# Optimization experiments

Hardware: AMD Instinct MI355X
Metric: run time of the kernel (lower is better)

## Reference

```python
import jax, jax.numpy as jnp
import numpy as np

B, N, C_IN, C_OUT, CHEB_K, EMB = 32, 2048, 128, 128, 3, 128
LN_EPS = 1e-12


def setup_inputs() -> dict:
    key = jax.random.key(0)
    k0, k1, k2, k3 = jax.random.split(key, 4)
    return {
        "x": jax.random.normal(k0, (B, N, C_IN), dtype=jnp.float32),
        "node_embeddings": jax.random.normal(k1, (N, EMB), dtype=jnp.float32),
        "weights_pool": jax.random.normal(k2, (EMB, CHEB_K, C_IN, C_OUT), dtype=jnp.float32) * 0.02,
        "bias_pool": jax.random.normal(k3, (EMB, C_OUT), dtype=jnp.float32) * 0.02,
        "ln_gamma": jnp.ones((EMB,), dtype=jnp.float32),
        "ln_beta": jnp.zeros((EMB,), dtype=jnp.float32),
    }


def reference(x, node_embeddings, weights_pool, bias_pool, ln_gamma, ln_beta):
    # x: [B, N, C_in]; node_embeddings: [N, D]
    cheb_k = weights_pool.shape[1]
    n = node_embeddings.shape[0]

    # LayerNorm over embed dim (biased variance, eps=1e-12); dropout is eval-mode identity
    mu = jnp.mean(node_embeddings, axis=-1, keepdims=True)
    var = jnp.mean(jnp.square(node_embeddings - mu), axis=-1, keepdims=True)
    e = (node_embeddings - mu) * jax.lax.rsqrt(var + LN_EPS) * ln_gamma + ln_beta

    # Adaptive adjacency: softmax(elu(E E^T)) over last dim (mask=None path)
    supports = jax.nn.softmax(jax.nn.elu(e @ e.T), axis=-1)  # [N, N]

    # Chebyshev polynomial set: T0=I, T1=A, Tk = 2A Tk-1 - Tk-2
    s_list = [jnp.eye(n, dtype=x.dtype), supports]
    for _ in range(2, cheb_k):
        s_list.append(2.0 * supports @ s_list[-1] - s_list[-2])
    S = jnp.stack(s_list, axis=0)  # [K, N, N]

    # Hypernetwork: per-node weights and bias
    weights = jnp.einsum("nd,dkio->nkio", e, weights_pool)  # [N, K, C_in, C_out]
    bias = e @ bias_pool  # [N, C_out]

    # Graph conv: gather neighborhoods per Chebyshev order, then per-node GEMM
    x_g = jnp.einsum("knm,bmc->bnkc", S, x)  # [B, N, K, C_in]
    out = jnp.einsum("bnki,nkio->bno", x_g, weights) + bias  # [B, N, C_out]
    return out
```

## Files before the change

### kernel.cpp

```cpp
#include <hip/hip_runtime.h>

#define DI __device__ __forceinline__

typedef unsigned short u16;
typedef short short8 __attribute__((ext_vector_type(8)));
typedef float f32x4 __attribute__((ext_vector_type(4)));
typedef u16 u16x4 __attribute__((ext_vector_type(4)));

#define NN 2048
#define CC 128
#define BB 32
#define DD 128
#define OO 128
#define KI 384
#define JJ 49152

DI u16 f2bf(float f) {
  union { float f; unsigned u; } v; v.f = f;
  return (u16)((v.u + 0x7fffu + ((v.u >> 16) & 1u)) >> 16);
}
DI float bf2f(u16 h) {
  union { unsigned u; float f; } v; v.u = ((unsigned)h) << 16;
  return v.f;
}

typedef __attribute__((address_space(3))) unsigned int lds_u32;
typedef __attribute__((address_space(1))) unsigned int glob_u32;

DI void gl16(const void* g, void* l) {
  __builtin_amdgcn_global_load_lds((const glob_u32*)g, (lds_u32*)l, 16, 0, 0);
}

__global__ __launch_bounds__(128)
void k_ln(const float* __restrict__ emb, const float* __restrict__ gam,
          const float* __restrict__ bet, float* __restrict__ e,
          u16* __restrict__ ehi, u16* __restrict__ elo) {
  __shared__ float s2[2], q2[2];
  const int n = blockIdx.x, t = threadIdx.x;
  const float v = emb[(size_t)n * DD + t];
  float s = v;
  #pragma unroll
  for (int off = 32; off; off >>= 1) s += __shfl_down(s, off);
  if ((t & 63) == 0) s2[t >> 6] = s;
  __syncthreads();
  const float mu = (s2[0] + s2[1]) * (1.f / 128.f);
  const float dv = v - mu;
  float q = dv * dv;
  #pragma unroll
  for (int off = 32; off; off >>= 1) q += __shfl_down(q, off);
  if ((t & 63) == 0) q2[t >> 6] = q;
  __syncthreads();
  const float var = (q2[0] + q2[1]) * (1.f / 128.f);
  const float ev = dv * rsqrtf(var + 1e-12f) * gam[t] + bet[t];
  e[(size_t)n * DD + t] = ev;
  const u16 hi = f2bf(ev);
  ehi[(size_t)n * DD + t] = hi;
  elo[(size_t)n * DD + t] = f2bf(ev - bf2f(hi));
}

__global__ __launch_bounds__(256, 2)
void k_zg(const u16* __restrict__ ehi, const u16* __restrict__ elo, float* __restrict__ Z) {
  __shared__ char smem[32768];
  const int t = threadIdx.x;
  const int w = t >> 6, l = t & 63;
  const int l15 = l & 15, kg = l >> 4;
  const int wr = (w >> 1) * 64, wc = (w & 1) * 64;
  const int row0 = blockIdx.x * 128, col0 = blockIdx.y * 128;

  f32x4 acc[4][4];
  #pragma unroll
  for (int i = 0; i < 4; ++i)
    #pragma unroll
    for (int j = 0; j < 4; ++j) { f32x4 z = {0.f, 0.f, 0.f, 0.f}; acc[i][j] = z; }

  const int ra = t >> 3, sa = t & 7;
  #pragma unroll 1
  for (int it = 0; it < 6; ++it) {
    const int term = it >> 1;
    const int k0 = (it & 1) * 64;
    const u16* As = (term == 2) ? elo : ehi;
    const u16* Bs = (term == 1) ? elo : ehi;
    __syncthreads();
    #pragma unroll
    for (int i = 0; i < 4; ++i) {
      const int r = i * 32 + ra;
      const int ss = sa ^ (r & 7);
      gl16(As + (size_t)(row0 + r) * DD + k0 + ss * 8, smem + i * 4096 + t * 16);
      gl16(Bs + (size_t)(col0 + r) * DD + k0 + ss * 8, smem + 16384 + i * 4096 + t * 16);
    }
    __syncthreads();
    short8 af[2][4], bfv[2][4];
    #pragma unroll
    for (int mt = 0; mt < 4; ++mt) {
      const int row = wr + mt * 16 + l15;
      #pragma unroll
      for (int ks = 0; ks < 2; ++ks) {
        const int sl = (ks * 4 + kg) ^ (row & 7);
        af[ks][mt] = *(const short8*)(smem + row * 128 + sl * 16);
      }
    }
    #pragma unroll
    for (int nt = 0; nt < 4; ++nt) {
      const int row = wc + nt * 16 + l15;
      #pragma unroll
      for (int ks = 0; ks < 2; ++ks) {
        const int sl = (ks * 4 + kg) ^ (row & 7);
        bfv[ks][nt] = *(const short8*)(smem + 16384 + row * 128 + sl * 16);
      }
    }
    #pragma unroll
    for (int ks = 0; ks < 2; ++ks)
      #pragma unroll
      for (int mt = 0; mt < 4; ++mt)
        #pragma unroll
        for (int nt = 0; nt < 4; ++nt)
          acc[mt][nt] = __builtin_amdgcn_mfma_f32_16x16x32_bf16(af[ks][mt], bfv[ks][nt], acc[mt][nt], 0, 0, 0);
  }
  #pragma unroll
  for (int mt = 0; mt < 4; ++mt) {
    const int n_ = row0 + wr + mt * 16 + kg * 4;
    #pragma unroll
    for (int nt = 0; nt < 4; ++nt) {
      const int m_ = col0 + wc + nt * 16 + l15;
      #pragma unroll
      for (int r = 0; r < 4; ++r) {
        const float v = acc[mt][nt][r];
        Z[(size_t)(n_ + r) * NN + m_] = (v > 0.f) ? v : expm1f(v);
      }
    }
  }
}

__global__ __launch_bounds__(256)
void k_sm(const float* __restrict__ Z, u16* __restrict__ Abf) {
  __shared__ float red[4];
  const int n = blockIdx.x, t = threadIdx.x, w = t >> 6;
  const float* zr = Z + (size_t)n * NN + t * 8;
  float4 v0 = *(const float4*)(zr);
  float4 v1 = *(const float4*)(zr + 4);
  float z[8] = {v0.x, v0.y, v0.z, v0.w, v1.x, v1.y, v1.z, v1.w};
  float mx = z[0];
  #pragma unroll
  for (int i = 1; i < 8; ++i) mx = fmaxf(mx, z[i]);
  #pragma unroll
  for (int off = 32; off; off >>= 1) mx = fmaxf(mx, __shfl_xor(mx, off));
  if ((t & 63) == 0) red[w] = mx;
  __syncthreads();
  mx = fmaxf(fmaxf(red[0], red[1]), fmaxf(red[2], red[3]));
  __syncthreads();
  float sm = 0.f;
  #pragma unroll
  for (int i = 0; i < 8; ++i) { z[i] = expf(z[i] - mx); sm += z[i]; }
  #pragma unroll
  for (int off = 32; off; off >>= 1) sm += __shfl_xor(sm, off);
  if ((t & 63) == 0) red[w] = sm;
  __syncthreads();
  const float inv = 1.f / (red[0] + red[1] + red[2] + red[3]);
  short8 pk;
  #pragma unroll
  for (int i = 0; i < 8; ++i) pk[i] = (short)f2bf(z[i] * inv);
  *(short8*)(Abf + (size_t)n * NN + t * 8) = pk;
}

__global__ __launch_bounds__(256)
void k_tc(const float* __restrict__ x, u16* __restrict__ xt, u16* __restrict__ xbf) {
  __shared__ float ld[64 * 68];
  const int t = threadIdx.x;
  const int m0 = blockIdx.x * 64, c0 = blockIdx.y * 64, b = blockIdx.z;
  const float* xb = x + (size_t)b * NN * CC;
  u16* xfb = xbf + (size_t)b * NN * CC;
  #pragma unroll
  for (int i = 0; i < 4; ++i) {
    const int m = i * 16 + (t >> 4), c4 = (t & 15) * 4;
    const float4 v = *(const float4*)&xb[(size_t)(m0 + m) * CC + c0 + c4];
    *(float4*)&ld[m * 68 + c4] = v;
    u16x4 cv = { f2bf(v.x), f2bf(v.y), f2bf(v.z), f2bf(v.w) };
    *(u16x4*)&xfb[(size_t)(m0 + m) * CC + c0 + c4] = cv;
  }
  __syncthreads();
  u16* xtb = xt + (size_t)b * CC * NN;
  #pragma unroll
  for (int i = 0; i < 4; ++i) {
    const int c = i * 16 + (t >> 4), m4 = (t & 15) * 4;
    u16x4 v = { f2bf(ld[(m4 + 0) * 68 + c]), f2bf(ld[(m4 + 1) * 68 + c]),
                f2bf(ld[(m4 + 2) * 68 + c]), f2bf(ld[(m4 + 3) * 68 + c]) };
    *(u16x4*)&xtb[(size_t)(c0 + c) * NN + m0 + m4] = v;
  }
}

__global__ __launch_bounds__(256)
void k_wpt(const float* __restrict__ wp, u16* __restrict__ wpt) {
  __shared__ float ld[64 * 68];
  const int t = threadIdx.x;
  const int d0 = blockIdx.x * 64, o0 = blockIdx.y * 64, ki = blockIdx.z;
  #pragma unroll
  for (int i = 0; i < 4; ++i) {
    const int d = i * 16 + (t >> 4), o4 = (t & 15) * 4;
    *(float4*)&ld[d * 68 + o4] = *(const float4*)&wp[((size_t)(d0 + d) * KI + ki) * OO + o0 + o4];
  }
  __syncthreads();
  #pragma unroll
  for (int i = 0; i < 4; ++i) {
    const int o = i * 16 + (t >> 4), d4 = (t & 15) * 4;
    u16x4 v = { f2bf(ld[(d4 + 0) * 68 + o]), f2bf(ld[(d4 + 1) * 68 + o]),
                f2bf(ld[(d4 + 2) * 68 + o]), f2bf(ld[(d4 + 3) * 68 + o]) };
    *(u16x4*)&wpt[((size_t)(o0 + o) * KI + ki) * DD + d0 + d4] = v;
  }
}

__global__ __launch_bounds__(128)
void k_bias(const float* __restrict__ e, const float* __restrict__ bp, float* __restrict__ bias) {
  const int n = blockIdx.x, o = threadIdx.x;
  const float* er = e + (size_t)n * DD;
  float acc = 0.f;
  for (int d = 0; d < 128; ++d) acc = fmaf(er[d], bp[(size_t)d * OO + o], acc);
  bias[(size_t)n * OO + o] = acc;
}

template<int MODE>
__global__ __launch_bounds__(256, 2)
void gemm_bf16(const u16* __restrict__ Ab, int lda,
               const u16* __restrict__ Bb, int ldb, int ksteps,
               u16* __restrict__ out0, u16* __restrict__ out1,
               const u16* __restrict__ xaux) {
  __shared__ char smem[34816];
  const int t = threadIdx.x;
  const int w = t >> 6, l = t & 63;
  const int l15 = l & 15, kg = l >> 4;
  const int wr = (w >> 1) * 64, wc = (w & 1) * 64;

  const u16 *Abase, *Bbase;
  int row0 = 0, col0 = 0, b = 0;
  if constexpr (MODE == 0 || MODE == 1) {
    const int lin = blockIdx.x + (int)gridDim.x * blockIdx.y;
    const int xcd = lin & 7, pos = lin >> 3;
    const int tile = xcd * 2 + (pos & 1);
    b = pos >> 1;
    if constexpr (MODE == 0) {
      row0 = tile * 128;
      Abase = Ab + (size_t)row0 * lda;
      Bbase = Bb + (size_t)b * CC * NN;
    } else {
      col0 = tile * 128;
      Abase = Ab + (size_t)b * CC * NN;
      Bbase = Bb + (size_t)col0 * NN;
    }
  } else {
    row0 = blockIdx.x * 128; col0 = blockIdx.y * 128;
    Abase = Ab + (size_t)row0 * 128;
    Bbase = Bb + (size_t)col0 * 128;
  }

  f32x4 acc[4][4];
  #pragma unroll
  for (int i = 0; i < 4; ++i)
    #pragma unroll
    for (int j = 0; j < 4; ++j) { f32x4 z = {0.f, 0.f, 0.f, 0.f}; acc[i][j] = z; }

  const int ra = t >> 3, sa = t & 7;
  for (int kt = 0; kt < ksteps; ++kt) {
    const int k0 = kt * 64;
    __syncthreads();
    #pragma unroll
    for (int i = 0; i < 4; ++i) {
      const int r = i * 32 + ra;
      const int ss = sa ^ (r & 7);
      gl16(Abase + (size_t)r * lda + k0 + ss * 8, smem + i * 4096 + t * 16);
    }
    #pragma unroll
    for (int i = 0; i < 4; ++i) {
      const int r = i * 32 + ra;
      const int ss = sa ^ (r & 7);
      gl16(Bbase + (size_t)r * ldb + k0 + ss * 8, smem + 16384 + i * 4096 + t * 16);
    }
    __syncthreads();
    short8 af[2][4], bfv[2][4];
    #pragma unroll
    for (int mt = 0; mt < 4; ++mt) {
      const int row = wr + mt * 16 + l15;
      #pragma unroll
      for (int ks = 0; ks < 2; ++ks) {
        const int sl = (ks * 4 + kg) ^ (row & 7);
        af[ks][mt] = *(const short8*)(smem + row * 128 + sl * 16);
      }
    }
    #pragma unroll
    for (int nt = 0; nt < 4; ++nt) {
      const int row = wc + nt * 16 + l15;
      #pragma unroll
      for (int ks = 0; ks < 2; ++ks) {
        const int sl = (ks * 4 + kg) ^ (row & 7);
        bfv[ks][nt] = *(const short8*)(smem + 16384 + row * 128 + sl * 16);
      }
    }
    #pragma unroll
    for (int ks = 0; ks < 2; ++ks)
      #pragma unroll
      for (int mt = 0; mt < 4; ++mt)
        #pragma unroll
        for (int nt = 0; nt < 4; ++nt)
          acc[mt][nt] = __builtin_amdgcn_mfma_f32_16x16x32_bf16(af[ks][mt], bfv[ks][nt], acc[mt][nt], 0, 0, 0);
  }

  if constexpr (MODE == 0) {
    u16* y1t = out0 + (size_t)b * CC * NN;
    #pragma unroll
    for (int mt = 0; mt < 4; ++mt) {
      const int n_ = row0 + wr + mt * 16 + kg * 4;
      #pragma unroll
      for (int nt = 0; nt < 4; ++nt) {
        const int c_ = wc + nt * 16 + l15;
        u16x4 v = { f2bf(acc[mt][nt][0]), f2bf(acc[mt][nt][1]),
                    f2bf(acc[mt][nt][2]), f2bf(acc[mt][nt][3]) };
        *(u16x4*)(y1t + (size_t)c_ * NN + n_) = v;
      }
    }
    __syncthreads();
    u16* L = (u16*)smem;
    #pragma unroll
    for (int mt = 0; mt < 4; ++mt) {
      const int nl = wr + mt * 16 + kg * 4;
      #pragma unroll
      for (int nt = 0; nt < 4; ++nt) {
        const int c_ = wc + nt * 16 + l15;
        #pragma unroll
        for (int r = 0; r < 4; ++r) L[(nl + r) * 136 + c_] = f2bf(acc[mt][nt][r]);
      }
    }
    __syncthreads();
    u16* y1o = out1 + (size_t)b * NN * CC;
    const int nl2 = t >> 1, ch = (t & 1) * 64;
    #pragma unroll
    for (int q = 0; q < 8; ++q) {
      short8 vv = *(const short8*)(L + nl2 * 136 + ch + q * 8);
      *(short8*)(y1o + (size_t)(row0 + nl2) * CC + ch + q * 8) = vv;
    }
  } else if constexpr (MODE == 1) {
    const u16* xb = xaux + (size_t)b * NN * CC;
    u16* y2b = out0 + (size_t)b * NN * CC;
    #pragma unroll
    for (int mt = 0; mt < 4; ++mt) {
      const int c_ = wr + mt * 16 + kg * 4;
      #pragma unroll
      for (int nt = 0; nt < 4; ++nt) {
        const int n_ = col0 + wc + nt * 16 + l15;
        const u16x4 xv = *(const u16x4*)(xb + (size_t)n_ * CC + c_);
        u16x4 v = { f2bf(2.f * acc[mt][nt][0] - bf2f(xv[0])),
                    f2bf(2.f * acc[mt][nt][1] - bf2f(xv[1])),
                    f2bf(2.f * acc[mt][nt][2] - bf2f(xv[2])),
                    f2bf(2.f * acc[mt][nt][3] - bf2f(xv[3])) };
        *(u16x4*)(y2b + (size_t)n_ * CC + c_) = v;
      }
    }
  } else {
    u16* wtb = out0 + (size_t)col0 * JJ;
    #pragma unroll
    for (int mt = 0; mt < 4; ++mt) {
      const int j_ = row0 + wr + mt * 16 + kg * 4;
      #pragma unroll
      for (int nt = 0; nt < 4; ++nt) {
        const int nl = wc + nt * 16 + l15;
        u16x4 v = { f2bf(acc[mt][nt][0]), f2bf(acc[mt][nt][1]),
                    f2bf(acc[mt][nt][2]), f2bf(acc[mt][nt][3]) };
        *(u16x4*)(wtb + (size_t)nl * JJ + j_) = v;
      }
    }
  }
}

__global__ __launch_bounds__(256, 4)
void stage_b(const u16* __restrict__ xbf, const u16* __restrict__ y1,
             const u16* __restrict__ y2, const u16* __restrict__ Wt,
             const float* __restrict__ bias, float* __restrict__ out, int nbase) {
  const int t = threadIdx.x, w = t >> 6, l = t & 63;
  const int l15 = l & 15, kg = l >> 4;
  const int n = nbase + blockIdx.x;
  const u16* Wn = Wt + (size_t)blockIdx.x * JJ;
  f32x4 acc[2][2];
  {
    f32x4 z = {0.f, 0.f, 0.f, 0.f};
    acc[0][0] = z; acc[0][1] = z; acc[1][0] = z; acc[1][1] = z;
  }
  #pragma unroll
  for (int ch2 = 0; ch2 < 3; ++ch2) {
    const u16* src = (ch2 == 0) ? xbf : (ch2 == 1) ? y1 : y2;
    #pragma unroll
    for (int ks = 0; ks < 4; ++ks) {
      short8 af[2];
      #pragma unroll
      for (int mt = 0; mt < 2; ++mt) {
        const int bb2 = mt * 16 + l15;
        af[mt] = *(const short8*)(src + ((size_t)bb2 * NN + n) * CC + ks * 32 + kg * 8);
      }
      #pragma unroll
      for (int ot = 0; ot < 2; ++ot) {
        const int o = w * 32 + ot * 16 + l15;
        const int ki = ch2 * 128 + ks * 32 + kg * 8;
        short8 bv = *(const short8*)(Wn + (size_t)o * KI + ki);
        acc[0][ot] = __builtin_amdgcn_mfma_f32_16x16x32_bf16(af[0], bv, acc[0][ot], 0, 0, 0);
        acc[1][ot] = __builtin_amdgcn_mfma_f32_16x16x32_bf16(af[1], bv, acc[1][ot], 0, 0, 0);
      }
    }
  }
  #pragma unroll
  for (int ot = 0; ot < 2; ++ot) {
    const int o = w * 32 + ot * 16 + l15;
    const float bs = bias[(size_t)n * OO + o];
    #pragma unroll
    for (int mt = 0; mt < 2; ++mt)
      #pragma unroll
      for (int r = 0; r < 4; ++r) {
        const int bb2 = mt * 16 + kg * 4 + r;
        out[((size_t)bb2 * NN + n) * OO + o] = acc[mt][ot][r] + bs;
      }
  }
}

extern "C" void kernel_launch(void* const* d_in, const int* in_sizes, int n_in,
                              void* d_out, int out_size, void* d_ws, size_t ws_size,
                              hipStream_t stream) {
  (void)in_sizes; (void)n_in; (void)out_size;
  const float* x   = (const float*)d_in[0];
  const float* emb = (const float*)d_in[1];
  const float* wp  = (const float*)d_in[2];
  const float* bp  = (const float*)d_in[3];
  const float* gam = (const float*)d_in[4];
  const float* bet = (const float*)d_in[5];
  float* out = (float*)d_out;
  char* ws = (char*)d_ws;

  size_t off = 0;
  auto alloc = [&](size_t bytes) -> void* {
    void* p = (void*)(ws + off);
    off += (bytes + 511) & ~(size_t)511;
    return p;
  };
  float* e    = (float*)alloc((size_t)NN * DD * 4);
  u16*   ehi  = (u16*)  alloc((size_t)NN * DD * 2);
  u16*   elo  = (u16*)  alloc((size_t)NN * DD * 2);
  float* bias = (float*)alloc((size_t)NN * OO * 4);
  u16*   Abf  = (u16*)  alloc((size_t)NN * NN * 2);
  u16*   xt   = (u16*)  alloc((size_t)BB * CC * NN * 2);
  u16*   xbf  = (u16*)  alloc((size_t)BB * NN * CC * 2);
  u16*   y1t  = (u16*)  alloc((size_t)BB * CC * NN * 2);
  u16*   y1   = (u16*)  alloc((size_t)BB * NN * CC * 2);
  u16*   y2   = (u16*)  alloc((size_t)BB * NN * CC * 2);
  u16*   wpt  = (u16*)  alloc((size_t)JJ * DD * 2);
  const size_t rem = (ws_size > off) ? (ws_size - off) : 0;
  int chunk = 1024;
  while (chunk > 128 && (size_t)chunk * JJ * 2 > rem) chunk >>= 1;
  u16* wt = (u16*)alloc((size_t)chunk * JJ * 2);
  float* Z = (float*)wt;

  k_ln<<<NN, 128, 0, stream>>>(emb, gam, bet, e, ehi, elo);
  k_zg<<<dim3(16, 16), 256, 0, stream>>>(ehi, elo, Z);
  k_sm<<<NN, 256, 0, stream>>>(Z, Abf);
  k_tc<<<dim3(NN / 64, CC / 64, BB), 256, 0, stream>>>(x, xt, xbf);
  k_wpt<<<dim3(2, 2, KI), 256, 0, stream>>>(wp, wpt);
  k_bias<<<NN, 128, 0, stream>>>(e, bp, bias);

  gemm_bf16<0><<<dim3(16, 32), 256, 0, stream>>>(Abf, NN, xt, NN, 32, y1t, y1, nullptr);
  gemm_bf16<1><<<dim3(16, 32), 256, 0, stream>>>(y1t, NN, Abf, NN, 32, y2, nullptr, xbf);

  for (int nb = 0; nb < NN; nb += chunk) {
    gemm_bf16<2><<<dim3(JJ / 128, chunk / 128), 256, 0, stream>>>(
        wpt, DD, ehi + (size_t)nb * DD, DD, 2, wt, nullptr, nullptr);
    stage_b<<<chunk, 256, 0, stream>>>(xbf, y1, y2, wt, bias, out, nb);
  }
}
```

Before: 382.1 us.

## Relayout per-node weight buffer for coalesced writes and use nontemporal stores

Changes the layout of the generated per-node weight tensor so the hypernetwork GEMM writes contiguous 128-element rows per (j-block, node), and stage_b reads with a matching strided index. Nontemporal stores are added across all intermediate and output writes to avoid polluting caches with streaming data. The workspace allocation is also fixed to guarantee room for the Z scratch matrix. The new layout changes the read pattern in stage_b, and nontemporal stores could hurt where later kernels re-read data that would otherwise have stayed in cache.

```diff
diff --git a/kernel.cpp b/kernel.cpp
--- a/kernel.cpp
+++ b/kernel.cpp
@@ -125,7 +125,8 @@
       #pragma unroll
       for (int r = 0; r < 4; ++r) {
         const float v = acc[mt][nt][r];
-        Z[(size_t)(n_ + r) * NN + m_] = (v > 0.f) ? v : expm1f(v);
+        __builtin_nontemporal_store((v > 0.f) ? v : expm1f(v),
+                                    Z + (size_t)(n_ + r) * NN + m_);
       }
     }
   }
@@ -175,7 +176,7 @@
     const float4 v = *(const float4*)&xb[(size_t)(m0 + m) * CC + c0 + c4];
     *(float4*)&ld[m * 68 + c4] = v;
     u16x4 cv = { f2bf(v.x), f2bf(v.y), f2bf(v.z), f2bf(v.w) };
-    *(u16x4*)&xfb[(size_t)(m0 + m) * CC + c0 + c4] = cv;
+    __builtin_nontemporal_store(cv, (u16x4*)&xfb[(size_t)(m0 + m) * CC + c0 + c4]);
   }
   __syncthreads();
   u16* xtb = xt + (size_t)b * CC * NN;
@@ -184,7 +185,7 @@
     const int c = i * 16 + (t >> 4), m4 = (t & 15) * 4;
     u16x4 v = { f2bf(ld[(m4 + 0) * 68 + c]), f2bf(ld[(m4 + 1) * 68 + c]),
                 f2bf(ld[(m4 + 2) * 68 + c]), f2bf(ld[(m4 + 3) * 68 + c]) };
-    *(u16x4*)&xtb[(size_t)(c0 + c) * NN + m0 + m4] = v;
+    __builtin_nontemporal_store(v, (u16x4*)&xtb[(size_t)(c0 + c) * NN + m0 + m4]);
   }
 }
 
@@ -204,7 +205,7 @@
     const int o = i * 16 + (t >> 4), d4 = (t & 15) * 4;
     u16x4 v = { f2bf(ld[(d4 + 0) * 68 + o]), f2bf(ld[(d4 + 1) * 68 + o]),
                 f2bf(ld[(d4 + 2) * 68 + o]), f2bf(ld[(d4 + 3) * 68 + o]) };
-    *(u16x4*)&wpt[((size_t)(o0 + o) * KI + ki) * DD + d0 + d4] = v;
+    __builtin_nontemporal_store(v, (u16x4*)&wpt[((size_t)(o0 + o) * KI + ki) * DD + d0 + d4]);
   }
 }
 
@@ -312,7 +313,7 @@
         const int c_ = wc + nt * 16 + l15;
         u16x4 v = { f2bf(acc[mt][nt][0]), f2bf(acc[mt][nt][1]),
                     f2bf(acc[mt][nt][2]), f2bf(acc[mt][nt][3]) };
-        *(u16x4*)(y1t + (size_t)c_ * NN + n_) = v;
+        __builtin_nontemporal_store(v, (u16x4*)(y1t + (size_t)c_ * NN + n_));
       }
     }
     __syncthreads();
@@ -333,7 +334,7 @@
     #pragma unroll
     for (int q = 0; q < 8; ++q) {
       short8 vv = *(const short8*)(L + nl2 * 136 + ch + q * 8);
-      *(short8*)(y1o + (size_t)(row0 + nl2) * CC + ch + q * 8) = vv;
+      __builtin_nontemporal_store(vv, (short8*)(y1o + (size_t)(row0 + nl2) * CC + ch + q * 8));
     }
   } else if constexpr (MODE == 1) {
     const u16* xb = xaux + (size_t)b * NN * CC;
@@ -349,20 +350,20 @@
                     f2bf(2.f * acc[mt][nt][1] - bf2f(xv[1])),
                     f2bf(2.f * acc[mt][nt][2] - bf2f(xv[2])),
                     f2bf(2.f * acc[mt][nt][3] - bf2f(xv[3])) };
-        *(u16x4*)(y2b + (size_t)n_ * CC + c_) = v;
+        __builtin_nontemporal_store(v, (u16x4*)(y2b + (size_t)n_ * CC + c_));
       }
     }
   } else {
-    u16* wtb = out0 + (size_t)col0 * JJ;
-    #pragma unroll
-    for (int mt = 0; mt < 4; ++mt) {
-      const int j_ = row0 + wr + mt * 16 + kg * 4;
+    u16* wtb = out0 + (size_t)(row0 >> 7) * ((size_t)gridDim.y << 14);
+    #pragma unroll
+    for (int mt = 0; mt < 4; ++mt) {
+      const int jl = wr + mt * 16 + kg * 4;
       #pragma unroll
       for (int nt = 0; nt < 4; ++nt) {
-        const int nl = wc + nt * 16 + l15;
+        const int nl = col0 + wc + nt * 16 + l15;
         u16x4 v = { f2bf(acc[mt][nt][0]), f2bf(acc[mt][nt][1]),
                     f2bf(acc[mt][nt][2]), f2bf(acc[mt][nt][3]) };
-        *(u16x4*)(wtb + (size_t)nl * JJ + j_) = v;
+        __builtin_nontemporal_store(v, (u16x4*)(wtb + (size_t)nl * 128 + jl));
       }
     }
   }
@@ -375,7 +376,8 @@
   const int t = threadIdx.x, w = t >> 6, l = t & 63;
   const int l15 = l & 15, kg = l >> 4;
   const int n = nbase + blockIdx.x;
-  const u16* Wn = Wt + (size_t)blockIdx.x * JJ;
+  const size_t pstride = (size_t)gridDim.x << 7;
+  const u16* Wn = Wt + (size_t)blockIdx.x * 128;
   f32x4 acc[2][2];
   {
     f32x4 z = {0.f, 0.f, 0.f, 0.f};
@@ -395,8 +397,7 @@
       #pragma unroll
       for (int ot = 0; ot < 2; ++ot) {
         const int o = w * 32 + ot * 16 + l15;
-        const int ki = ch2 * 128 + ks * 32 + kg * 8;
-        short8 bv = *(const short8*)(Wn + (size_t)o * KI + ki);
+        short8 bv = *(const short8*)(Wn + (size_t)(3 * o + ch2) * pstride + ks * 32 + kg * 8);
         acc[0][ot] = __builtin_amdgcn_mfma_f32_16x16x32_bf16(af[0], bv, acc[0][ot], 0, 0, 0);
         acc[1][ot] = __builtin_amdgcn_mfma_f32_16x16x32_bf16(af[1], bv, acc[1][ot], 0, 0, 0);
       }
@@ -411,7 +412,8 @@
       #pragma unroll
       for (int r = 0; r < 4; ++r) {
         const int bb2 = mt * 16 + kg * 4 + r;
-        out[((size_t)bb2 * NN + n) * OO + o] = acc[mt][ot][r] + bs;
+        __builtin_nontemporal_store(acc[mt][ot][r] + bs,
+                                    out + ((size_t)bb2 * NN + n) * OO + o);
       }
   }
 }
@@ -449,7 +451,9 @@
   const size_t rem = (ws_size > off) ? (ws_size - off) : 0;
   int chunk = 1024;
   while (chunk > 128 && (size_t)chunk * JJ * 2 > rem) chunk >>= 1;
-  u16* wt = (u16*)alloc((size_t)chunk * JJ * 2);
+  size_t wt_bytes = (size_t)chunk * JJ * 2;
+  const size_t z_bytes = (size_t)NN * NN * 4;
+  u16* wt = (u16*)alloc(wt_bytes > z_bytes ? wt_bytes : z_bytes);
   float* Z = (float*)wt;
 
   k_ln<<<NN, 128, 0, stream>>>(emb, gam, bet, e, ehi, elo);
```

New measurement: 561.0 us. 46.8% more time.
